# Kernel optimization log

Measured on AMD Instinct MI355X. Metric: run time of the kernel, lower is better.

Reference implementation:

```python
import jax, jax.numpy as jnp
import numpy as np

BN_EPS = 1e-5

def _l2norm(x, axis):
    # F.normalize: x / max(||x||_2, 1e-12)
    n = jnp.sqrt(jnp.sum(x * x, axis=axis, keepdims=True))
    return x / jnp.maximum(n, 1e-12)

def _psi(x_bhc, w, g, b):
    # 1x1 conv over HW-as-channels: [B,HW,C] x [D,HW] -> [B,D,C]
    y = jnp.einsum('dh,bhc->bdc', w, x_bhc)
    # inference BatchNorm2d with running_mean=0, running_var=1
    scale = g / jnp.sqrt(1.0 + BN_EPS)
    y = y * scale[None, :, None] + b[None, :, None]
    return jax.nn.relu(y)

def setup_inputs() -> dict:
    key = jax.random.key(0)
    ks = jax.random.split(key, 8)
    B, C, H, W, D = 16, 2048, 32, 32, 256
    return {
        'v2l_conv_feature': jax.random.normal(ks[0], (B, C, H, W), jnp.float32),
        'l2v_conv_feature': jax.random.normal(ks[1], (B, C, H, W), jnp.float32),
        'w_v2l': jax.random.normal(ks[2], (D, H * W), jnp.float32) * 0.02,
        'g_v2l': jax.random.uniform(ks[3], (D,), jnp.float32, 0.5, 1.5),
        'b_v2l': jax.random.normal(ks[4], (D,), jnp.float32) * 0.1,
        'w_l2v': jax.random.normal(ks[5], (D, H * W), jnp.float32) * 0.02,
        'g_l2v': jax.random.uniform(ks[6], (D,), jnp.float32, 0.5, 1.5),
        'b_l2v': jax.random.normal(ks[7], (D,), jnp.float32) * 0.1,
    }

def reference(v2l_conv_feature, l2v_conv_feature, w_v2l, g_v2l, b_v2l, w_l2v, g_l2v, b_l2v):
    B, C, H, W = v2l_conv_feature.shape
    HW = H * W
    xv = jnp.transpose(v2l_conv_feature.reshape(B, C, HW), (0, 2, 1))  # [B,HW,C]
    xl = jnp.transpose(l2v_conv_feature.reshape(B, C, HW), (0, 2, 1))  # [B,HW,C]
    v2l_adj = _l2norm(_psi(xv, w_v2l, g_v2l, b_v2l), axis=2)  # [B,D,C], norm over C
    l2v_adj = _l2norm(_psi(xl, w_l2v, g_l2v, b_l2v), axis=1)  # [B,D,C], norm over D
    # Faithful to torch: reshape of the permuted tensor is a raw row-major
    # reinterpretation [B,HW,C] -> [B,C,HW] (NOT a transpose back).
    xv_r = xv.reshape(B, C, HW)
    latent = jnp.einsum('bdc,bch->bdh', v2l_adj, xv_r)          # [B,D,HW]
    latent_n = _l2norm(latent, axis=-1)
    aff = jax.nn.softmax(jnp.einsum('bdh,beh->bde', latent_n, latent_n), axis=-1)  # [B,D,D]
    latent = jnp.einsum('bde,beh->bdh', aff, latent)            # [B,D,HW]
    visible = jnp.einsum('bdc,bdh->bch', l2v_adj, latent)       # [B,C,HW]
    return visible.reshape(B, C, H, W)
```

## Files before the change

kernel.cpp:

```cpp
#include <hip/hip_runtime.h>
#include <hip/hip_bf16.h>

#define BB 16
#define CC 2048
#define HWW 1024
#define DD 256
#define BN_RSQRT 0.9999950000374997f

typedef short bf16x8 __attribute__((ext_vector_type(8)));
typedef float f32x4 __attribute__((ext_vector_type(4)));
typedef unsigned short u16x8 __attribute__((ext_vector_type(8)));
typedef unsigned short u16x4 __attribute__((ext_vector_type(4)));
typedef unsigned short u16;

typedef __attribute__((address_space(1))) const unsigned GU;
typedef __attribute__((address_space(3))) unsigned LU;
__device__ __forceinline__ void gload16(const void* g, void* l) {
    __builtin_amdgcn_global_load_lds((GU*)g, (LU*)l, 16, 0, 0);
}

__device__ __forceinline__ unsigned short f2bf(float x) {
    unsigned u = __builtin_bit_cast(unsigned, x);
    unsigned r = u + 0x7FFFu + ((u >> 16) & 1u);
    return (unsigned short)(r >> 16);
}
__device__ __forceinline__ float bf2f(unsigned short h) {
    unsigned u = ((unsigned)h) << 16;
    return __builtin_bit_cast(float, u);
}
__device__ __forceinline__ void split2(float x, unsigned short& hi, unsigned short& lo) {
    hi = f2bf(x);
    lo = f2bf(x - bf2f(hi));
}

struct RegsA { u16x8 h[2]; u16x8 l[2]; };
struct RegsB { u16x8 h[2]; u16x8 l[2]; };

__global__ __launch_bounds__(256) void split_k(const float* __restrict__ in,
                                               u16* __restrict__ hi, u16* __restrict__ lo,
                                               long long n8) {
    long long i = (long long)blockIdx.x * 256 + threadIdx.x;
    if (i >= n8) return;
    const float4* p = (const float4*)in + i * 2;
    float4 a = p[0], b = p[1];
    float xs[8] = {a.x, a.y, a.z, a.w, b.x, b.y, b.z, b.w};
    u16x8 h, l;
    #pragma unroll
    for (int j = 0; j < 8; ++j) { unsigned short hh, ll; split2(xs[j], hh, ll); h[j] = hh; l[j] = ll; }
    *(u16x8*)(hi + i * 8) = h;
    *(u16x8*)(lo + i * 8) = l;
}

template <int BF, int EPI, int FUSE2, int KS, int AT>
__global__ __launch_bounds__(512, 4) void gemm2b(
    const u16* __restrict__ Ah0, const u16* __restrict__ Al0,
    const u16* __restrict__ Ah1, const u16* __restrict__ Al1,
    long long aB, int lda,
    const void* __restrict__ B0a, const void* __restrict__ B0b,
    const void* __restrict__ B1a, const void* __restrict__ B1b,
    long long bB, int ldb,
    float* __restrict__ C0, float* __restrict__ C1,
    long long cB, long long kB, int ldc,
    int K,
    const float* __restrict__ g0, const float* __restrict__ bb0,
    const float* __restrict__ g1, const float* __restrict__ bb1)
{
    __shared__ __attribute__((aligned(16))) char smem[2][32768];

    const int gx = gridDim.x, gy = gridDim.y;
    int nwg = gx * gy * gridDim.z;
    int id = blockIdx.x + gx * (blockIdx.y + gy * blockIdx.z);
    int chunk = nwg >> 3;
    int nid = (id & 7) * chunk + (id >> 3);
    int bx = nid % gx;
    int tmp = nid / gx;
    int by = tmp % gy;
    int bz = tmp / gy;

    const int t = threadIdx.x;
    const int n0 = bx * 128, m0 = by * 128;

    int op = 0, batch, kz = 0;
    if constexpr (FUSE2) { op = bz >> 4; batch = bz & 15; }
    else if constexpr (KS > 1) { batch = bz / KS; kz = bz - batch * KS; }
    else { batch = bz; }
    const int koffA = kz * K;

    const u16* Ahp = (op ? Ah1 : Ah0) + (long long)batch * aB + (AT ? 0 : koffA);
    const u16* Alp = (op ? Al1 : Al0) + (long long)batch * aB + (AT ? 0 : koffA);
    const float* Bf = nullptr;
    const u16* Bh = nullptr;
    const u16* Bl = nullptr;
    if constexpr (BF == 0) {
        Bf = (const float*)(op ? B1a : B0a) + (long long)batch * bB;
        Bf += ((long long)(koffA >> 10)) * 1024 * ldb + (koffA & 1023);
    } else {
        Bh = (const u16*)(op ? B1a : B0a) + (long long)batch * bB;
        Bl = (const u16*)(op ? B1b : B0b) + (long long)batch * bB;
    }
    float* Cb = ((EPI == 1 && FUSE2) ? (op ? C1 : C0) : C0)
              + (long long)batch * cB + (long long)kz * kB;
    const float* gp = op ? g1 : g0;
    const float* bp = op ? bb1 : bb0;

    const int arow = t >> 2;
    const int aslt = (t & 3) ^ ((t >> 3) & 3);
    const int bswz = (t & 3) ^ ((arow >> 1) & 3);

    const int l = t & 63, w = t >> 6;
    const int wr = w >> 2, wc = w & 3;
    const int rl = l & 15, kq = l >> 4;
    const int fsw = (kq ^ ((rl >> 1) & 3)) * 16;

    f32x4 acc[4][2];
    #pragma unroll
    for (int i = 0; i < 4; ++i)
        #pragma unroll
        for (int j = 0; j < 2; ++j)
            acc[i][j] = (f32x4){0.f, 0.f, 0.f, 0.f};

    float4 rb0, rb1;

    auto loadBregs = [&](int k0) {
        if constexpr (BF == 0) {
            const float* p = Bf + (long long)(n0 + arow) * ldb + k0 + (t & 3) * 8;
            rb0 = *(const float4*)p;
            rb1 = *(const float4*)(p + 4);
        }
    };
    auto gstage = [&](int k0, char* sn) {
        if constexpr (AT == 1) {
            long long tb = (long long)((koffA + k0) >> 5) * 8192;
            const u16* pa = Ahp + tb + (m0 + arow) * 32 + aslt * 8;
            gload16(pa, sn + t * 16);
            const u16* pl = Alp + tb + (m0 + arow) * 32 + aslt * 8;
            gload16(pl, sn + 8192 + t * 16);
        } else {
            const u16* pa = Ahp + (long long)(m0 + arow) * lda + k0 + aslt * 8;
            gload16(pa, sn + t * 16);
            const u16* pl = Alp + (long long)(m0 + arow) * lda + k0 + aslt * 8;
            gload16(pl, sn + 8192 + t * 16);
        }
        if constexpr (BF == 1) {
            const u16* pbh = Bh + (long long)(n0 + arow) * ldb + k0 + aslt * 8;
            gload16(pbh, sn + 16384 + t * 16);
            const u16* pbl = Bl + (long long)(n0 + arow) * ldb + k0 + aslt * 8;
            gload16(pbl, sn + 24576 + t * 16);
        }
    };
    auto splitWriteB = [&](char* sn) {
        if constexpr (BF == 0) {
            float xs[8] = {rb0.x, rb0.y, rb0.z, rb0.w, rb1.x, rb1.y, rb1.z, rb1.w};
            u16x8 h, lo;
            #pragma unroll
            for (int e = 0; e < 8; ++e) {
                unsigned short hh, ll; split2(xs[e], hh, ll);
                h[e] = hh; lo[e] = ll;
            }
            char* base = sn + 16384 + arow * 64 + bswz * 16;
            *(u16x8*)(base) = h;
            *(u16x8*)(base + 8192) = lo;
        }
    };

    auto readA = [&](const char* sb, bf16x8* fah, bf16x8* fal) {
        #pragma unroll
        for (int i2 = 0; i2 < 4; ++i2) {
            int off = (wr * 64 + i2 * 16 + rl) * 64 + fsw;
            fah[i2] = *(const bf16x8*)(sb + off);
            fal[i2] = *(const bf16x8*)(sb + 8192 + off);
        }
    };
    auto readB = [&](const char* sb, bf16x8* fbh, bf16x8* fbl) {
        #pragma unroll
        for (int j = 0; j < 2; ++j) {
            int off = (wc * 32 + j * 16 + rl) * 64 + fsw;
            fbh[j] = *(const bf16x8*)(sb + 16384 + off);
            fbl[j] = *(const bf16x8*)(sb + 24576 + off);
        }
    };

    const int NIT = K >> 5;

    loadBregs(0);
    gstage(0, smem[0]);
    if constexpr (BF == 0) {
        asm volatile("s_waitcnt vmcnt(2)" ::: "memory");
        splitWriteB(smem[0]);
    }
    asm volatile("s_waitcnt vmcnt(0)" ::: "memory");
    asm volatile("s_waitcnt lgkmcnt(0)" ::: "memory");
    __builtin_amdgcn_s_barrier();

    for (int it = 0; it < NIT; ++it) {
        char* sb = smem[it & 1];
        char* sn = smem[(it + 1) & 1];
        const bool more = (it + 1) < NIT;
        if (more) { loadBregs((it + 1) << 5); gstage((it + 1) << 5, sn); }

        bf16x8 fah[4], fal[4], fbh[2], fbl[2];
        readB(sb, fbh, fbl);
        readA(sb, fah, fal);

        if (more && BF == 0) {
            asm volatile("s_waitcnt vmcnt(2)" ::: "memory");
            splitWriteB(sn);
        }

        __builtin_amdgcn_s_setprio(1);
        #pragma unroll
        for (int i2 = 0; i2 < 4; ++i2)
            #pragma unroll
            for (int j = 0; j < 2; ++j)
                acc[i2][j] = __builtin_amdgcn_mfma_f32_16x16x32_bf16(fal[i2], fbh[j], acc[i2][j], 0, 0, 0);
        #pragma unroll
        for (int i2 = 0; i2 < 4; ++i2)
            #pragma unroll
            for (int j = 0; j < 2; ++j)
                acc[i2][j] = __builtin_amdgcn_mfma_f32_16x16x32_bf16(fah[i2], fbl[j], acc[i2][j], 0, 0, 0);
        #pragma unroll
        for (int i2 = 0; i2 < 4; ++i2)
            #pragma unroll
            for (int j = 0; j < 2; ++j)
                acc[i2][j] = __builtin_amdgcn_mfma_f32_16x16x32_bf16(fah[i2], fbh[j], acc[i2][j], 0, 0, 0);
        __builtin_amdgcn_s_setprio(0);

        if (more) { asm volatile("s_waitcnt vmcnt(0)" ::: "memory"); }
        asm volatile("s_waitcnt lgkmcnt(0)" ::: "memory");
        __builtin_amdgcn_s_barrier();
    }

    #pragma unroll
    for (int i = 0; i < 4; ++i) {
        #pragma unroll
        for (int r = 0; r < 4; ++r) {
            int row = m0 + wr * 64 + i * 16 + kq * 4 + r;
            float sc = 1.0f, bi = 0.0f;
            if (EPI == 1) { sc = gp[row] * BN_RSQRT; bi = bp[row]; }
            #pragma unroll
            for (int j = 0; j < 2; ++j) {
                int col = n0 + wc * 32 + j * 16 + rl;
                float v = acc[i][j][r];
                if (EPI == 1) v = fmaxf(fmaf(v, sc, bi), 0.0f);
                Cb[(long long)row * ldc + col] = v;
            }
        }
    }
}

template <int BN_, int EPI>
__global__ __launch_bounds__(256) void mfma_gemm(
    const void* __restrict__ Ap, const void* __restrict__ Ap2, long long aB, int lda,
    const void* __restrict__ Bp, const void* __restrict__ Bp2, long long bB, int ldb,
    void* __restrict__ Cp, void* __restrict__ Cp2,
    long long cB, int ldc, int K)
{
    constexpr int NJ   = BN_ / 32;
    constexpr int BNB  = BN_ * 64;
    constexpr int BUFB = 16384 + BN_ * 128;
    __shared__ __attribute__((aligned(16))) char smem[2][BUFB];

    const int gx = gridDim.x, gy = gridDim.y;
    int nwg = gx * gy * gridDim.z;
    int id = blockIdx.x + gx * (blockIdx.y + gy * blockIdx.z);
    int chunk = nwg >> 3;
    int nid = (id & 7) * chunk + (id >> 3);
    int bx = nid % gx;
    int tmp = nid / gx;
    int by = tmp % gy;
    int bz = tmp / gy;

    const int t  = threadIdx.x;
    const int n0 = bx * BN_;
    const int m0 = by * 128;

    const int ar = t >> 1, ag = t & 1;
    const int af = (ar >> 1) & 3;
    const int as0 = (2 * ag) ^ af, as1 = (2 * ag + 1) ^ af;
    const bool bact = (BN_ == 128) || (t < 2 * BN_);
    const int br = (t >> 1) & (BN_ - 1), bg = t & 1;
    const int bf = (br >> 1) & 3;
    const int bs0 = (2 * bg) ^ bf, bs1 = (2 * bg + 1) ^ bf;

    const int l  = t & 63, w = t >> 6;
    const int wr = w >> 1, wc = w & 1;
    const int rl = l & 15, kq = l >> 4;
    const int sw = kq ^ ((rl >> 1) & 3);
    const int aoff = (wr * 64 + rl) * 64 + sw * 16;
    const int boff = (wc * (BN_ / 2) + rl) * 64 + sw * 16;

    const u16* Ahp = (const u16*)Ap  + (long long)bz * aB;
    const u16* Alp = (const u16*)Ap2 + (long long)bz * aB;
    const u16* Bhp = (const u16*)Bp  + (long long)bz * bB;
    const u16* Blp = (const u16*)Bp2 + (long long)bz * bB;

    auto loadA = [&](int k0, RegsA& ra) {
        const u16* ph = Ahp + (long long)(m0 + ar) * lda + k0 + ag * 16;
        const u16* pl = Alp + (long long)(m0 + ar) * lda + k0 + ag * 16;
        ra.h[0] = *(const u16x8*)(ph);
        ra.h[1] = *(const u16x8*)(ph + 8);
        ra.l[0] = *(const u16x8*)(pl);
        ra.l[1] = *(const u16x8*)(pl + 8);
    };
    auto loadB = [&](int k0, RegsB& rb) {
        if (!bact) return;
        const u16* ph = Bhp + (long long)(n0 + br) * ldb + k0 + bg * 16;
        const u16* pl = Blp + (long long)(n0 + br) * ldb + k0 + bg * 16;
        rb.h[0] = *(const u16x8*)(ph);
        rb.h[1] = *(const u16x8*)(ph + 8);
        rb.l[0] = *(const u16x8*)(pl);
        rb.l[1] = *(const u16x8*)(pl + 8);
    };
    auto stageWrite = [&](char* sb, RegsA& ra, RegsB& rb) {
        *(u16x8*)(sb + ar * 64 + as0 * 16) = ra.h[0];
        *(u16x8*)(sb + ar * 64 + as1 * 16) = ra.h[1];
        *(u16x8*)(sb + 8192 + ar * 64 + as0 * 16) = ra.l[0];
        *(u16x8*)(sb + 8192 + ar * 64 + as1 * 16) = ra.l[1];
        if (bact) {
            char* sB = sb + 16384;
            *(u16x8*)(sB + br * 64 + bs0 * 16) = rb.h[0];
            *(u16x8*)(sB + br * 64 + bs1 * 16) = rb.h[1];
            *(u16x8*)(sB + BNB + br * 64 + bs0 * 16) = rb.l[0];
            *(u16x8*)(sB + BNB + br * 64 + bs1 * 16) = rb.l[1];
        }
    };

    f32x4 acc[4][NJ];
    #pragma unroll
    for (int i = 0; i < 4; ++i)
        #pragma unroll
        for (int j = 0; j < NJ; ++j)
            acc[i][j] = (f32x4){0.f, 0.f, 0.f, 0.f};

    RegsA a0, a1;
    RegsB b0, b1;
    const int NIT = K >> 5;

    loadA(0, a0); loadB(0, b0);
    stageWrite(smem[0], a0, b0);
    loadA(32, a1); loadB(32, b1);
    asm volatile("s_waitcnt lgkmcnt(0)" ::: "memory");
    __builtin_amdgcn_s_barrier();

    auto step = [&](int it, char* sb, char* sn, RegsA& pa, RegsB& pb,
                    RegsA& qa, RegsB& qb) {
        bf16x8 fah[4], fal[4], fbh[NJ], fbl[NJ];
        #pragma unroll
        for (int i = 0; i < 4; ++i) {
            fah[i] = *(const bf16x8*)(sb + aoff + i * 1024);
            fal[i] = *(const bf16x8*)(sb + 8192 + aoff + i * 1024);
        }
        #pragma unroll
        for (int j = 0; j < NJ; ++j) {
            fbh[j] = *(const bf16x8*)(sb + 16384 + boff + j * 1024);
            fbl[j] = *(const bf16x8*)(sb + 16384 + BNB + boff + j * 1024);
        }
        if (it + 1 < NIT) stageWrite(sn, pa, pb);
        if (it + 2 < NIT) { loadA((it + 2) << 5, qa); loadB((it + 2) << 5, qb); }
        #pragma unroll
        for (int i = 0; i < 4; ++i)
            #pragma unroll
            for (int j = 0; j < NJ; ++j) {
                acc[i][j] = __builtin_amdgcn_mfma_f32_16x16x32_bf16(fal[i], fbh[j], acc[i][j], 0, 0, 0);
                acc[i][j] = __builtin_amdgcn_mfma_f32_16x16x32_bf16(fah[i], fbl[j], acc[i][j], 0, 0, 0);
                acc[i][j] = __builtin_amdgcn_mfma_f32_16x16x32_bf16(fah[i], fbh[j], acc[i][j], 0, 0, 0);
            }
        asm volatile("s_waitcnt lgkmcnt(0)" ::: "memory");
        __builtin_amdgcn_s_barrier();
    };

    for (int it = 0; it < NIT; it += 2) {
        step(it,     smem[0], smem[1], a1, b1, a0, b0);
        step(it + 1, smem[1], smem[0], a0, b0, a1, b1);
    }

    #pragma unroll
    for (int i = 0; i < 4; ++i) {
        #pragma unroll
        for (int r = 0; r < 4; ++r) {
            int row = m0 + wr * 64 + i * 16 + kq * 4 + r;
            #pragma unroll
            for (int j = 0; j < NJ; ++j) {
                int col = n0 + wc * (BN_ / 2) + j * 16 + rl;
                float v = acc[i][j][r];
                if constexpr (EPI == 0) {
                    ((float*)Cp + (long long)bz * cB)[(long long)row * ldc + col] = v;
                } else {
                    unsigned short hh, ll; split2(v, hh, ll);
                    ((u16*)Cp  + (long long)bz * cB)[(long long)row * ldc + col] = hh;
                    ((u16*)Cp2 + (long long)bz * cB)[(long long)row * ldc + col] = ll;
                }
            }
        }
    }
}

__global__ __launch_bounds__(256) void rownorm_split_tiled_k(const float* __restrict__ Y,
                                                             u16* __restrict__ T) {
    int d = blockIdx.x, b = blockIdx.y, t = threadIdx.x;
    const float* row = Y + ((long long)b * DD + d) * CC;
    float4 v0 = ((const float4*)row)[2 * t];
    float4 v1 = ((const float4*)row)[2 * t + 1];
    float s = v0.x * v0.x + v0.y * v0.y + v0.z * v0.z + v0.w * v0.w
            + v1.x * v1.x + v1.y * v1.y + v1.z * v1.z + v1.w * v1.w;
    for (int off = 32; off > 0; off >>= 1) s += __shfl_down(s, off, 64);
    __shared__ float wsum[4];
    __shared__ float ivs;
    int lane = t & 63, w = t >> 6;
    if (lane == 0) wsum[w] = s;
    __syncthreads();
    if (t == 0) ivs = 1.0f / fmaxf(sqrtf(wsum[0] + wsum[1] + wsum[2] + wsum[3]), 1e-12f);
    __syncthreads();
    float iv = ivs;
    float xs[8] = {v0.x * iv, v0.y * iv, v0.z * iv, v0.w * iv,
                   v1.x * iv, v1.y * iv, v1.z * iv, v1.w * iv};
    u16x4 he, ho, le, lo4;
    #pragma unroll
    for (int j = 0; j < 4; ++j) {
        unsigned short hh, ll;
        split2(xs[2 * j], hh, ll);       he[j] = hh; le[j] = ll;
        split2(xs[2 * j + 1], hh, ll);   ho[j] = hh; lo4[j] = ll;
    }
    u16* Tb = T + (long long)b * 1048576;
    int kk  = 4 * (t & 7);
    long long oE = ((long long)(t >> 3) * 256 + d) * 32 + kk;
    long long oO = ((long long)(32 + (t >> 3)) * 256 + d) * 32 + kk;
    *(u16x4*)(Tb + oE) = he;
    *(u16x4*)(Tb + oO) = ho;
    *(u16x4*)(Tb + 524288 + oE) = le;
    *(u16x4*)(Tb + 524288 + oO) = lo4;
}

__global__ __launch_bounds__(256) void transnorm_k(const float* __restrict__ Yl,
                                                   u16* __restrict__ hi, u16* __restrict__ lo) {
    __shared__ float tile[256][33];
    __shared__ float part[8][33];
    __shared__ float invn[32];
    int c0 = blockIdx.x * 32, b = blockIdx.y;
    int t = threadIdx.x;
    int tx = t & 31, ty = t >> 5;
    const float* base = Yl + (long long)b * DD * CC + c0;
    for (int d = ty; d < 256; d += 8)
        tile[d][tx] = base[(long long)d * CC + tx];
    __syncthreads();
    float s = 0.0f;
    #pragma unroll
    for (int dd = 0; dd < 32; ++dd) {
        float v = tile[ty * 32 + dd][tx];
        s += v * v;
    }
    part[ty][tx] = s;
    __syncthreads();
    if (ty == 0) {
        float tot = part[0][tx] + part[1][tx] + part[2][tx] + part[3][tx]
                  + part[4][tx] + part[5][tx] + part[6][tx] + part[7][tx];
        invn[tx] = 1.0f / fmaxf(sqrtf(tot), 1e-12f);
    }
    __syncthreads();
    long long ob = (long long)b * DD * CC;
    #pragma unroll 4
    for (int i = 0; i < 32; ++i) {
        float v = tile[t][i] * invn[i];
        unsigned short hh, ll; split2(v, hh, ll);
        long long o = ob + (long long)(c0 + i) * DD + t;
        hi[o] = hh; lo[o] = ll;
    }
}

__global__ __launch_bounds__(256) void latreduce_k(const float* __restrict__ parts,
                                                   u16* __restrict__ hi, u16* __restrict__ lo,
                                                   u16* __restrict__ thi, u16* __restrict__ tlo) {
    __shared__ float tile[32][33];
    int h0 = blockIdx.x * 32, d0 = blockIdx.y * 32, b = blockIdx.z;
    const long long sL = (long long)DD * HWW;
    const long long ps = (long long)BB * sL;
    const float* base = parts + (long long)b * sL;
    int tx = threadIdx.x & 31, ty = threadIdx.x >> 5;
    for (int i = ty; i < 32; i += 8) {
        long long o = (long long)(d0 + i) * HWW + h0 + tx;
        float s = base[o] + base[o + ps];
        tile[i][tx] = s;
        unsigned short hh, ll; split2(s, hh, ll);
        long long od = (long long)b * sL + o;
        hi[od] = hh; lo[od] = ll;
    }
    __syncthreads();
    for (int i = ty; i < 32; i += 8) {
        float v = tile[tx][i];
        unsigned short hh, ll; split2(v, hh, ll);
        long long ot = (long long)b * sL + (long long)(h0 + i) * DD + d0 + tx;
        thi[ot] = hh; tlo[ot] = ll;
    }
}

__global__ __launch_bounds__(256) void latnorm_k(const float* __restrict__ G,
                                                 float* __restrict__ rs) {
    int i = blockIdx.x * 256 + threadIdx.x;
    int b = i >> 8, d = i & 255;
    float v = G[((long long)b * DD + d) * DD + d];
    rs[i] = 1.0f / fmaxf(sqrtf(v), 1e-12f);
}

__global__ __launch_bounds__(256) void softmax_k(const float* __restrict__ G,
                                                 const float* __restrict__ rs,
                                                 u16* __restrict__ affHi,
                                                 u16* __restrict__ affLo) {
    int d = blockIdx.x, b = blockIdx.y;
    const float* row = G + ((long long)b * DD + d) * DD;
    const float* rsb = rs + (long long)b * DD;
    int t = threadIdx.x;
    float lg = row[t] * rsb[d] * rsb[t];

    float m = lg;
    for (int off = 32; off > 0; off >>= 1) m = fmaxf(m, __shfl_down(m, off, 64));
    __shared__ float wsm[4];
    __shared__ float bm, bs;
    int lane = t & 63, w = t >> 6;
    if (lane == 0) wsm[w] = m;
    __syncthreads();
    if (t == 0) bm = fmaxf(fmaxf(wsm[0], wsm[1]), fmaxf(wsm[2], wsm[3]));
    __syncthreads();
    float e = expf(lg - bm);
    float s = e;
    for (int off = 32; off > 0; off >>= 1) s += __shfl_down(s, off, 64);
    if (lane == 0) wsm[w] = s;
    __syncthreads();
    if (t == 0) bs = wsm[0] + wsm[1] + wsm[2] + wsm[3];
    __syncthreads();
    float v = e / bs;
    unsigned short hh, ll; split2(v, hh, ll);
    long long o = ((long long)b * DD + d) * DD + t;
    affHi[o] = hh; affLo[o] = ll;
}

extern "C" void kernel_launch(void* const* d_in, const int* in_sizes, int n_in,
                              void* d_out, int out_size, void* d_ws, size_t ws_size,
                              hipStream_t stream) {
    const float* v2l   = (const float*)d_in[0];
    const float* l2v   = (const float*)d_in[1];
    const float* w_v2l = (const float*)d_in[2];
    const float* g_v2l = (const float*)d_in[3];
    const float* b_v2l = (const float*)d_in[4];
    const float* w_l2v = (const float*)d_in[5];
    const float* g_l2v = (const float*)d_in[6];
    const float* b_l2v = (const float*)d_in[7];
    float* out = (float*)d_out;

    char* W = (char*)d_ws;
    float* Yv     = (float*)(W + 0);
    float* Yl     = (float*)(W + 33554432);
    u16*   YltHi  = (u16*)(W + 67108864);
    u16*   YltLo  = (u16*)(W + 83886080);
    u16*   latHi  = (u16*)(W + 100663296);
    u16*   latLo  = (u16*)(W + 109051904);
    u16*   latTHi = (u16*)(W + 117440512);
    u16*   latTLo = (u16*)(W + 125829120);
    u16*   l2tHi  = (u16*)(W + 134217728);
    u16*   l2tLo  = (u16*)(W + 142606336);
    float* gram   = (float*)(W + 150994944);
    float* rs     = (float*)(W + 155189248);
    u16*   affHi  = (u16*)(W + 155336704);
    u16*   affLo  = (u16*)(W + 157433856);
    u16*   WvHi   = (u16*)(W + 159531008);
    u16*   WvLo   = WvHi + 262144;
    u16*   WlHi   = WvLo + 262144;
    u16*   WlLo   = WlHi + 262144;

    float* latPart = (float*)d_out;
    u16*   YvT     = (u16*)((char*)d_out + 67108864);

    const long long sY   = (long long)DD * CC;
    const long long sL   = (long long)DD * HWW;
    const long long sG   = (long long)DD * DD;
    const long long sX   = (long long)CC * HWW;

    split_k<<<128, 256, 0, stream>>>(w_v2l, WvHi, WvLo, 32768);
    split_k<<<128, 256, 0, stream>>>(w_l2v, WlHi, WlLo, 32768);

    gemm2b<0, 1, 1, 1, 0><<<dim3(CC / 128, DD / 128, 32), 512, 0, stream>>>(
        WvHi, WvLo, WlHi, WlLo, 0, HWW,
        v2l, nullptr, l2v, nullptr, sX, HWW,
        Yv, Yl, sY, 0, CC, HWW,
        g_v2l, b_v2l, g_l2v, b_l2v);

    rownorm_split_tiled_k<<<dim3(DD, BB), 256, 0, stream>>>(Yv, YvT);
    transnorm_k<<<dim3(CC / 32, BB), 256, 0, stream>>>(Yl, YltHi, YltLo);

    gemm2b<0, 0, 0, 2, 1><<<dim3(HWW / 128, DD / 128, 32), 512, 0, stream>>>(
        YvT, YvT + 524288, nullptr, nullptr, 1048576, 32,
        v2l, nullptr, nullptr, nullptr, sX, HWW,
        latPart, nullptr, sL, (long long)BB * sL, HWW, 1024,
        nullptr, nullptr, nullptr, nullptr);

    latreduce_k<<<dim3(HWW / 32, DD / 32, BB), 256, 0, stream>>>(
        latPart, latHi, latLo, latTHi, latTLo);

    mfma_gemm<64, 0><<<dim3(4, 2, BB), 256, 0, stream>>>(
        latHi, latLo, sL, HWW, latHi, latLo, sL, HWW,
        gram, nullptr, sG, DD, HWW);

    latnorm_k<<<dim3(BB * DD / 256), 256, 0, stream>>>(gram, rs);
    softmax_k<<<dim3(DD, BB), 256, 0, stream>>>(gram, rs, affHi, affLo);

    mfma_gemm<128, 2><<<dim3(2, 8, BB), 256, 0, stream>>>(
        latTHi, latTLo, sL, DD, affHi, affLo, sG, DD,
        l2tHi, l2tLo, sL, DD, DD);

    gemm2b<1, 0, 0, 1, 0><<<dim3(HWW / 128, CC / 128, BB), 512, 0, stream>>>(
        YltHi, YltLo, nullptr, nullptr, sY, DD,
        l2tHi, l2tLo, nullptr, nullptr, sL, DD,
        out, nullptr, sX, 0, HWW, DD,
        nullptr, nullptr, nullptr, nullptr);
}
```

Baseline: 349.5 us.

## Pre-convert input features to bf16 and drop lo-part MFMA pass in GEMMs

Result: no change. 354.9 us (+1.6%).

```diff
diff --git a/kernel.cpp b/kernel.cpp
--- a/kernel.cpp
+++ b/kernel.cpp
@@ -51,7 +51,19 @@
     *(u16x8*)(lo + i * 8) = l;
 }
 
-template <int BF, int EPI, int FUSE2, int KS, int AT>
+__global__ __launch_bounds__(256) void shi_k(const float* __restrict__ in,
+                                             u16* __restrict__ hi, long long n8) {
+    long long i = (long long)blockIdx.x * 256 + threadIdx.x;
+    if (i >= n8) return;
+    const float4* p = (const float4*)in + i * 2;
+    float4 a = p[0], b = p[1];
+    u16x8 h;
+    h[0] = f2bf(a.x); h[1] = f2bf(a.y); h[2] = f2bf(a.z); h[3] = f2bf(a.w);
+    h[4] = f2bf(b.x); h[5] = f2bf(b.y); h[6] = f2bf(b.z); h[7] = f2bf(b.w);
+    *(u16x8*)(hi + i * 8) = h;
+}
+
+template <int EPI, int FUSE2, int KS, int AT, int BL>
 __global__ __launch_bounds__(512, 4) void gemm2b(
     const u16* __restrict__ Ah0, const u16* __restrict__ Al0,
     const u16* __restrict__ Ah1, const u16* __restrict__ Al1,
@@ -65,7 +77,8 @@
     const float* __restrict__ g0, const float* __restrict__ bb0,
     const float* __restrict__ g1, const float* __restrict__ bb1)
 {
-    __shared__ __attribute__((aligned(16))) char smem[2][32768];
+    constexpr int BUFB = (BL == 1) ? 32768 : 24576;
+    __shared__ __attribute__((aligned(16))) char smem[2][BUFB];
 
     const int gx = gridDim.x, gy = gridDim.y;
     int nwg = gx * gy * gridDim.z;
@@ -88,16 +101,10 @@
 
     const u16* Ahp = (op ? Ah1 : Ah0) + (long long)batch * aB + (AT ? 0 : koffA);
     const u16* Alp = (op ? Al1 : Al0) + (long long)batch * aB + (AT ? 0 : koffA);
-    const float* Bf = nullptr;
-    const u16* Bh = nullptr;
+    const u16* Bh = (const u16*)(op ? B1a : B0a) + (long long)batch * bB;
     const u16* Bl = nullptr;
-    if constexpr (BF == 0) {
-        Bf = (const float*)(op ? B1a : B0a) + (long long)batch * bB;
-        Bf += ((long long)(koffA >> 10)) * 1024 * ldb + (koffA & 1023);
-    } else {
-        Bh = (const u16*)(op ? B1a : B0a) + (long long)batch * bB;
-        Bl = (const u16*)(op ? B1b : B0b) + (long long)batch * bB;
-    }
+    if constexpr (BL == 1) Bl = (const u16*)(op ? B1b : B0b) + (long long)batch * bB;
+    if constexpr (KS > 1) Bh += (long long)kz * 1024 * ldb;
     float* Cb = ((EPI == 1 && FUSE2) ? (op ? C1 : C0) : C0)
               + (long long)batch * cB + (long long)kz * kB;
     const float* gp = op ? g1 : g0;
@@ -105,7 +112,6 @@
 
     const int arow = t >> 2;
     const int aslt = (t & 3) ^ ((t >> 3) & 3);
-    const int bswz = (t & 3) ^ ((arow >> 1) & 3);
 
     const int l = t & 63, w = t >> 6;
     const int wr = w >> 2, wc = w & 3;
@@ -119,48 +125,18 @@
         for (int j = 0; j < 2; ++j)
             acc[i][j] = (f32x4){0.f, 0.f, 0.f, 0.f};
 
-    float4 rb0, rb1;
-
-    auto loadBregs = [&](int k0) {
-        if constexpr (BF == 0) {
-            const float* p = Bf + (long long)(n0 + arow) * ldb + k0 + (t & 3) * 8;
-            rb0 = *(const float4*)p;
-            rb1 = *(const float4*)(p + 4);
-        }
-    };
     auto gstage = [&](int k0, char* sn) {
         if constexpr (AT == 1) {
             long long tb = (long long)((koffA + k0) >> 5) * 8192;
-            const u16* pa = Ahp + tb + (m0 + arow) * 32 + aslt * 8;
-            gload16(pa, sn + t * 16);
-            const u16* pl = Alp + tb + (m0 + arow) * 32 + aslt * 8;
-            gload16(pl, sn + 8192 + t * 16);
+            gload16(Ahp + tb + (m0 + arow) * 32 + aslt * 8, sn + t * 16);
+            gload16(Alp + tb + (m0 + arow) * 32 + aslt * 8, sn + 8192 + t * 16);
         } else {
-            const u16* pa = Ahp + (long long)(m0 + arow) * lda + k0 + aslt * 8;
-            gload16(pa, sn + t * 16);
-            const u16* pl = Alp + (long long)(m0 + arow) * lda + k0 + aslt * 8;
-            gload16(pl, sn + 8192 + t * 16);
-        }
-        if constexpr (BF == 1) {
-            const u16* pbh = Bh + (long long)(n0 + arow) * ldb + k0 + aslt * 8;
-            gload16(pbh, sn + 16384 + t * 16);
-            const u16* pbl = Bl + (long long)(n0 + arow) * ldb + k0 + aslt * 8;
-            gload16(pbl, sn + 24576 + t * 16);
-        }
-    };
-    auto splitWriteB = [&](char* sn) {
-        if constexpr (BF == 0) {
-            float xs[8] = {rb0.x, rb0.y, rb0.z, rb0.w, rb1.x, rb1.y, rb1.z, rb1.w};
-            u16x8 h, lo;
-            #pragma unroll
-            for (int e = 0; e < 8; ++e) {
-                unsigned short hh, ll; split2(xs[e], hh, ll);
-                h[e] = hh; lo[e] = ll;
-            }
-            char* base = sn + 16384 + arow * 64 + bswz * 16;
-            *(u16x8*)(base) = h;
-            *(u16x8*)(base + 8192) = lo;
-        }
+            gload16(Ahp + (long long)(m0 + arow) * lda + k0 + aslt * 8, sn + t * 16);
+            gload16(Alp + (long long)(m0 + arow) * lda + k0 + aslt * 8, sn + 8192 + t * 16);
+        }
+        gload16(Bh + (long long)(n0 + arow) * ldb + k0 + aslt * 8, sn + 16384 + t * 16);
+        if constexpr (BL == 1)
+            gload16(Bl + (long long)(n0 + arow) * ldb + k0 + aslt * 8, sn + 24576 + t * 16);
     };
 
     auto readA = [&](const char* sb, bf16x8* fah, bf16x8* fal) {
@@ -176,36 +152,25 @@
         for (int j = 0; j < 2; ++j) {
             int off = (wc * 32 + j * 16 + rl) * 64 + fsw;
             fbh[j] = *(const bf16x8*)(sb + 16384 + off);
-            fbl[j] = *(const bf16x8*)(sb + 24576 + off);
+            if constexpr (BL == 1) fbl[j] = *(const bf16x8*)(sb + 24576 + off);
         }
     };
 
     const int NIT = K >> 5;
 
-    loadBregs(0);
     gstage(0, smem[0]);
-    if constexpr (BF == 0) {
-        asm volatile("s_waitcnt vmcnt(2)" ::: "memory");
-        splitWriteB(smem[0]);
-    }
     asm volatile("s_waitcnt vmcnt(0)" ::: "memory");
-    asm volatile("s_waitcnt lgkmcnt(0)" ::: "memory");
     __builtin_amdgcn_s_barrier();
 
     for (int it = 0; it < NIT; ++it) {
         char* sb = smem[it & 1];
         char* sn = smem[(it + 1) & 1];
         const bool more = (it + 1) < NIT;
-        if (more) { loadBregs((it + 1) << 5); gstage((it + 1) << 5, sn); }
+        if (more) gstage((it + 1) << 5, sn);
 
         bf16x8 fah[4], fal[4], fbh[2], fbl[2];
         readB(sb, fbh, fbl);
         readA(sb, fah, fal);
-
-        if (more && BF == 0) {
-            asm volatile("s_waitcnt vmcnt(2)" ::: "memory");
-            splitWriteB(sn);
-        }
 
         __builtin_amdgcn_s_setprio(1);
         #pragma unroll
@@ -213,11 +178,13 @@
             #pragma unroll
             for (int j = 0; j < 2; ++j)
                 acc[i2][j] = __builtin_amdgcn_mfma_f32_16x16x32_bf16(fal[i2], fbh[j], acc[i2][j], 0, 0, 0);
-        #pragma unroll
-        for (int i2 = 0; i2 < 4; ++i2)
+        if constexpr (BL == 1) {
             #pragma unroll
-            for (int j = 0; j < 2; ++j)
-                acc[i2][j] = __builtin_amdgcn_mfma_f32_16x16x32_bf16(fah[i2], fbl[j], acc[i2][j], 0, 0, 0);
+            for (int i2 = 0; i2 < 4; ++i2)
+                #pragma unroll
+                for (int j = 0; j < 2; ++j)
+                    acc[i2][j] = __builtin_amdgcn_mfma_f32_16x16x32_bf16(fah[i2], fbl[j], acc[i2][j], 0, 0, 0);
+        }
         #pragma unroll
         for (int i2 = 0; i2 < 4; ++i2)
             #pragma unroll
@@ -546,9 +513,14 @@
     const float* b_l2v = (const float*)d_in[7];
     float* out = (float*)d_out;
 
+    u16* v2lH = (u16*)d_out;
+    u16* l2vH = (u16*)((char*)d_out + 67108864);
+    u16* YvT  = (u16*)((char*)d_out + 67108864);
+
     char* W = (char*)d_ws;
     float* Yv     = (float*)(W + 0);
     float* Yl     = (float*)(W + 33554432);
+    float* latPart= (float*)(W + 0);
     u16*   YltHi  = (u16*)(W + 67108864);
     u16*   YltLo  = (u16*)(W + 83886080);
     u16*   latHi  = (u16*)(W + 100663296);
@@ -566,9 +538,6 @@
     u16*   WlHi   = WvLo + 262144;
     u16*   WlLo   = WlHi + 262144;
 
-    float* latPart = (float*)d_out;
-    u16*   YvT     = (u16*)((char*)d_out + 67108864);
-
     const long long sY   = (long long)DD * CC;
     const long long sL   = (long long)DD * HWW;
     const long long sG   = (long long)DD * DD;
@@ -576,19 +545,21 @@
 
     split_k<<<128, 256, 0, stream>>>(w_v2l, WvHi, WvLo, 32768);
     split_k<<<128, 256, 0, stream>>>(w_l2v, WlHi, WlLo, 32768);
-
-    gemm2b<0, 1, 1, 1, 0><<<dim3(CC / 128, DD / 128, 32), 512, 0, stream>>>(
+    shi_k<<<16384, 256, 0, stream>>>(v2l, v2lH, 4194304);
+    shi_k<<<16384, 256, 0, stream>>>(l2v, l2vH, 4194304);
+
+    gemm2b<1, 1, 1, 0, 0><<<dim3(CC / 128, DD / 128, 32), 512, 0, stream>>>(
         WvHi, WvLo, WlHi, WlLo, 0, HWW,
-        v2l, nullptr, l2v, nullptr, sX, HWW,
+        v2lH, nullptr, l2vH, nullptr, sX, HWW,
         Yv, Yl, sY, 0, CC, HWW,
         g_v2l, b_v2l, g_l2v, b_l2v);
 
     rownorm_split_tiled_k<<<dim3(DD, BB), 256, 0, stream>>>(Yv, YvT);
     transnorm_k<<<dim3(CC / 32, BB), 256, 0, stream>>>(Yl, YltHi, YltLo);
 
-    gemm2b<0, 0, 0, 2, 1><<<dim3(HWW / 128, DD / 128, 32), 512, 0, stream>>>(
+    gemm2b<0, 0, 2, 1, 0><<<dim3(HWW / 128, DD / 128, 32), 512, 0, stream>>>(
         YvT, YvT + 524288, nullptr, nullptr, 1048576, 32,
-        v2l, nullptr, nullptr, nullptr, sX, HWW,
+        v2lH, nullptr, nullptr, nullptr, sX, HWW,
         latPart, nullptr, sL, (long long)BB * sL, HWW, 1024,
         nullptr, nullptr, nullptr, nullptr);
 
@@ -606,7 +577,7 @@
         latTHi, latTLo, sL, DD, affHi, affLo, sG, DD,
         l2tHi, l2tLo, sL, DD, DD);
 
-    gemm2b<1, 0, 0, 1, 0><<<dim3(HWW / 128, CC / 128, BB), 512, 0, stream>>>(
+    gemm2b<0, 0, 1, 0, 1><<<dim3(HWW / 128, CC / 128, BB), 512, 0, stream>>>(
         YltHi, YltLo, nullptr, nullptr, sY, DD,
         l2tHi, l2tLo, nullptr, nullptr, sL, DD,
         out, nullptr, sX, 0, HWW, DD,
```
